# Performance work log

Hardware: AMD Instinct MI355X
Metric: run time of the kernel (lower is better)

## Reference

```python
import jax, jax.numpy as jnp
import numpy as np

THRESH = 1.0        # cif_weight_threshold
MAX_HIST = 10       # max_history
RELU_THRESH = 1.0   # relu_threshold (crelu clip)
NORM_SCALAR = 1.0   # normalize_scalar


def setup_inputs() -> dict:
    key = jax.random.key(0)
    k0, k1, k2 = jax.random.split(key, 3)
    B, T, H = 32, 2048, 256
    encoder_outputs = jax.random.normal(k0, (B, T, H), jnp.float32)
    mask = jnp.ones((B, 200, 1), jnp.float32)
    W1 = jax.random.normal(k1, (2 * H, 2 * H), jnp.float32) * 0.02
    b1 = jnp.zeros((2 * H,), jnp.float32)
    W2 = jax.random.normal(k2, (1, 2 * H), jnp.float32) * 0.02
    b2 = jnp.zeros((1,), jnp.float32)
    return {"encoder_outputs": encoder_outputs, "mask": mask,
            "W1": W1, "b1": b1, "W2": W2, "b2": b2, "is_training": 1}


def _cif_forward(x, mask, W1, b1, W2, b2, is_training):
    B, T, H = x.shape
    dt = x.dtype
    # number of non-zero (effective) frames per utterance
    first_pad = jnp.sum((jnp.sum(jnp.abs(x), -1) != 0.0).astype(jnp.int32), 1)  # [B]

    # ---- history chunk: mean over window [max(0, t-MAX_HIST), t); t==0 uses x[:,0] ----
    cs = jnp.concatenate([jnp.zeros((B, 1, H), dt), jnp.cumsum(x, axis=1)], axis=1)  # [B,T+1,H]
    t_idx = jnp.arange(T)
    start = jnp.maximum(0, t_idx - MAX_HIST)
    count = jnp.maximum(t_idx - start, 1).astype(dt)
    hist = (cs[:, t_idx, :] - cs[:, start, :]) / count[None, :, None]     # [B,T,H]
    hist = jnp.where((t_idx == 0)[None, :, None], x[:, 0:1, :], hist)

    # ---- weight prediction (two dense layers, crelu + clip) ----
    info = jnp.concatenate([x, x - hist], axis=-1)                        # [B,T,2H]
    h = jnp.einsum('btc,oc->bto', info, W1) + b1
    w = (jnp.einsum('btc,oc->bto', h, W2) + b2)[..., 0]                   # [B,T]
    w = jnp.clip(jax.nn.relu(w), None, RELU_THRESH)
    ori_weight = w
    sum_a = w.sum(1)

    if is_training:  # static python int; using_scaling=True, mask provided
        N = mask[:, :, 0].sum(-1) - 1.0
        scale = N / jnp.clip(sum_a, 1e-8)
        scale = jnp.where(sum_a == 0, jnp.zeros_like(sum_a), scale)
        w = scale[:, None] * w

    pad_mask = t_idx[None, :] > first_pad[:, None]                        # [B,T]
    w = jnp.where(pad_mask, 0.0, w)

    # ---- accumulate-and-fire scan ----
    def step(carry, inp):
        prev_w, prev_s = carry
        w_t, x_t = inp                                                    # [B], [B,H]
        fired = prev_w + w_t > THRESH
        remained = THRESH - prev_w
        new_w = jnp.where(fired, w_t - remained, w_t + prev_w)
        integ = prev_s + (1.0 - w_t)[:, None] * x_t
        new_s = jnp.where(fired[:, None], x_t, integ)
        fired_s = jnp.where(fired[:, None], integ, jnp.zeros_like(integ))
        return (new_w, new_s), (fired, fired_s)

    init = (jnp.zeros((B,), dt), x[:, 0, :])
    (fin_w, fin_s), (fired_flags, fired_states) = jax.lax.scan(
        step, init, (w.T, jnp.swapaxes(x, 0, 1)))

    fired_states = jnp.swapaxes(fired_states, 0, 1)                       # [B,T,H]
    fired_flag = fired_flags.T[:, :, None].astype(dt)                     # [B,T,1]
    fired_states = jnp.where(pad_mask[:, :, None], 0.0, fired_states)
    fired_states = jnp.concatenate([fired_states, fin_s[:, None, :]], 1)  # [B,T+1,H] (tail)

    # ---- compact fired states to the front (torch truncates to max fired len;
    #      here we keep fixed length T+1 and pad with zeros, which is a superset) ----
    L = T + 1
    fired_marks = (jnp.sum(jnp.abs(fired_states), -1) != 0.0).astype(jnp.int32)
    pos = jnp.cumsum(fired_marks, axis=1) - 1
    pos = jnp.where(fired_marks == 1, pos, L)  # out-of-bounds -> dropped
    cif = jnp.zeros((B, L, H), dt)
    cif = cif.at[jnp.arange(B)[:, None], pos].set(fired_states, mode='drop')

    not_padding_after_cif = (jnp.sum(jnp.abs(cif), -1) != 0.0).astype(jnp.int32)
    norm = jnp.linalg.norm(cif, axis=-1, keepdims=True)
    cif = NORM_SCALAR * cif / jnp.maximum(norm, 1e-12)  # F.normalize(p=2)
    return cif, ori_weight, fired_flag, not_padding_after_cif, sum_a


def reference(encoder_outputs, mask, W1, b1, W2, b2, is_training):
    return _cif_forward(encoder_outputs, mask, W1, b1, W2, b2, is_training)
```

## Files before the change

### kernel.cpp

```cpp
#include <hip/hip_runtime.h>

#define B_ 32
#define T_ 2048
#define H_ 256
#define L_ 2049

__device__ inline double waveReduceD(double v) {
#pragma unroll
  for (int off = 32; off > 0; off >>= 1) v += __shfl_xor(v, off, 64);
  return v;
}

typedef float vfloat4 __attribute__((ext_vector_type(4)));
__device__ inline void nt_store4(float4 v, float* p) {
  vfloat4 t;
  t.x = v.x; t.y = v.y; t.z = v.z; t.w = v.w;
  __builtin_nontemporal_store(t, (vfloat4*)p);
}

__global__ void __launch_bounds__(256) k0_fold(
    const float* __restrict__ W1, const float* __restrict__ b1,
    const float* __restrict__ W2, const float* __restrict__ b2,
    double* __restrict__ vd, double* __restrict__ c0) {
  __shared__ double s_p[8][32];
  int tid = threadIdx.x;
  int cl = tid & 31, sl = tid >> 5;
  int c = blockIdx.x * 32 + cl;
  double acc = 0.0;
#pragma unroll 8
  for (int o = sl * 64; o < sl * 64 + 64; ++o)
    acc += (double)W2[o] * (double)W1[o * 512 + c];
  s_p[sl][cl] = acc;
  __syncthreads();
  if (sl == 0) {
    double v = 0.0;
#pragma unroll
    for (int i = 0; i < 8; ++i) v += s_p[i][cl];
    vd[c] = v;
  }
  if (blockIdx.x == 0) {
    __shared__ double red[256];
    double p = (double)W2[tid] * (double)b1[tid] +
               (double)W2[tid + 256] * (double)b1[tid + 256];
    red[tid] = p;
    __syncthreads();
    for (int s = 128; s > 0; s >>= 1) {
      if (tid < s) red[tid] += red[tid + s];
      __syncthreads();
    }
    if (tid == 0) c0[0] = red[0] + (double)b2[0];
  }
}

__global__ void __launch_bounds__(256) k1_rowdots(
    const float* __restrict__ x, const double* __restrict__ vd,
    double* __restrict__ d1, double* __restrict__ d2, float* __restrict__ absS) {
  int wave = threadIdx.x >> 6, lane = threadIdx.x & 63;
  long row0 = ((long)blockIdx.x * 4 + wave) * 4;
  const float4* xr = (const float4*)(x + row0 * H_);
  float4 x0 = xr[lane];
  float4 x1 = xr[lane + 64];
  float4 x2 = xr[lane + 128];
  float4 x3 = xr[lane + 192];
  int base = lane * 4;
  double vb0 = vd[256 + base + 0], vb1 = vd[256 + base + 1],
         vb2 = vd[256 + base + 2], vb3 = vd[256 + base + 3];
  double va0 = vd[base + 0] + vb0, va1 = vd[base + 1] + vb1,
         va2 = vd[base + 2] + vb2, va3 = vd[base + 3] + vb3;
  double p10 = (double)x0.x * va0 + (double)x0.y * va1 + (double)x0.z * va2 + (double)x0.w * va3;
  double p20 = (double)x0.x * vb0 + (double)x0.y * vb1 + (double)x0.z * vb2 + (double)x0.w * vb3;
  double p11 = (double)x1.x * va0 + (double)x1.y * va1 + (double)x1.z * va2 + (double)x1.w * va3;
  double p21 = (double)x1.x * vb0 + (double)x1.y * vb1 + (double)x1.z * vb2 + (double)x1.w * vb3;
  double p12 = (double)x2.x * va0 + (double)x2.y * va1 + (double)x2.z * va2 + (double)x2.w * va3;
  double p22 = (double)x2.x * vb0 + (double)x2.y * vb1 + (double)x2.z * vb2 + (double)x2.w * vb3;
  double p13 = (double)x3.x * va0 + (double)x3.y * va1 + (double)x3.z * va2 + (double)x3.w * va3;
  double p23 = (double)x3.x * vb0 + (double)x3.y * vb1 + (double)x3.z * vb2 + (double)x3.w * vb3;
  bool n0 = (x0.x != 0.0f) || (x0.y != 0.0f) || (x0.z != 0.0f) || (x0.w != 0.0f);
  bool n1 = (x1.x != 0.0f) || (x1.y != 0.0f) || (x1.z != 0.0f) || (x1.w != 0.0f);
  bool n2 = (x2.x != 0.0f) || (x2.y != 0.0f) || (x2.z != 0.0f) || (x2.w != 0.0f);
  bool n3 = (x3.x != 0.0f) || (x3.y != 0.0f) || (x3.z != 0.0f) || (x3.w != 0.0f);
  unsigned long long b0 = __ballot(n0), b1_ = __ballot(n1),
                     b2_ = __ballot(n2), b3 = __ballot(n3);
#pragma unroll
  for (int off = 32; off > 0; off >>= 1) {
    p10 += __shfl_xor(p10, off, 64);
    p20 += __shfl_xor(p20, off, 64);
    p11 += __shfl_xor(p11, off, 64);
    p21 += __shfl_xor(p21, off, 64);
    p12 += __shfl_xor(p12, off, 64);
    p22 += __shfl_xor(p22, off, 64);
    p13 += __shfl_xor(p13, off, 64);
    p23 += __shfl_xor(p23, off, 64);
  }
  if (lane == 0)       { d1[row0 + 0] = p10; d2[row0 + 0] = p20; absS[row0 + 0] = b0  ? 1.0f : 0.0f; }
  else if (lane == 16) { d1[row0 + 1] = p11; d2[row0 + 1] = p21; absS[row0 + 1] = b1_ ? 1.0f : 0.0f; }
  else if (lane == 32) { d1[row0 + 2] = p12; d2[row0 + 2] = p22; absS[row0 + 2] = b2_ ? 1.0f : 0.0f; }
  else if (lane == 48) { d1[row0 + 3] = p13; d2[row0 + 3] = p23; absS[row0 + 3] = b3  ? 1.0f : 0.0f; }
}

__global__ void __launch_bounds__(256) k2_weights(
    const double* __restrict__ d1, const double* __restrict__ d2,
    const float* __restrict__ absS, const float* __restrict__ mask,
    const int* __restrict__ is_tr, const double* __restrict__ c0p,
    float* __restrict__ o_ori, float* __restrict__ o_sa, float* __restrict__ o_ff,
    float* __restrict__ wsc, int* __restrict__ fireT,
    int* __restrict__ nAllArr, int* __restrict__ nUnmArr) {
  __shared__ double s_P[T_];
  __shared__ double s_tot[4];
  __shared__ double s_red[4][3];
  __shared__ double s_tot2[4];
  __shared__ double s_mtot[4];
  __shared__ int s_int[2];
  int b = blockIdx.x, tid = threadIdx.x;
  int lane = tid & 63, wv = tid >> 6;
  int t0 = tid * 8;
  const double* d1b = d1 + (long)b * T_;
  const double* d2b = d2 + (long)b * T_;
  const float* asb = absS + (long)b * T_;
  double c0 = c0p[0];

  double r2[8];
  {
    double run2 = 0.0;
#pragma unroll
    for (int k = 0; k < 8; ++k) { run2 += d2b[t0 + k]; r2[k] = run2; }
    double sc2 = run2;
#pragma unroll
    for (int off = 1; off < 64; off <<= 1) {
      double n = __shfl_up(sc2, off, 64);
      if (lane >= off) sc2 += n;
    }
    if (lane == 63) s_tot[wv] = sc2;
    __syncthreads();
    double base2 = 0.0;
    for (int i = 0; i < wv; ++i) base2 += s_tot[i];
    double e2 = base2 + (sc2 - run2);
#pragma unroll
    for (int k = 0; k < 8; ++k) s_P[t0 + k] = e2 + r2[k];
  }
  __syncthreads();

  double wd[8];
  double sa = 0.0, fpc = 0.0;
#pragma unroll
  for (int k = 0; k < 8; ++k) {
    int t = t0 + k;
    double wvv;
    if (t == 0) {
      wvv = d1b[0] - s_P[0] + c0;
    } else {
      int start = t - 10; if (start < 0) start = 0;
      double ws_ = s_P[t - 1] - (start > 0 ? s_P[start - 1] : 0.0);
      wvv = d1b[t] - ws_ / (double)(t - start) + c0;
    }
    wvv = wvv < 0.0 ? 0.0 : (wvv > 1.0 ? 1.0 : wvv);
    wd[k] = wvv;
    sa += wvv;
    fpc += (asb[t] != 0.0f) ? 1.0 : 0.0;
  }
  {
    float4* ov = (float4*)(o_ori + (long)b * T_ + t0);
    ov[0] = make_float4((float)wd[0], (float)wd[1], (float)wd[2], (float)wd[3]);
    ov[1] = make_float4((float)wd[4], (float)wd[5], (float)wd[6], (float)wd[7]);
  }
  double ms = (tid < 200) ? (double)mask[(long)b * 200 + tid] : 0.0;
  double sar = waveReduceD(sa), fpr = waveReduceD(fpc), msr = waveReduceD(ms);
  if (lane == 0) { s_red[wv][0] = sar; s_red[wv][1] = fpr; s_red[wv][2] = msr; }
  __syncthreads();
  double sumA = s_red[0][0] + s_red[1][0] + s_red[2][0] + s_red[3][0];
  double fpD  = s_red[0][1] + s_red[1][1] + s_red[2][1] + s_red[3][1];
  double maskSum = s_red[0][2] + s_red[1][2] + s_red[2][2] + s_red[3][2];
  if (tid == 0) o_sa[b] = (float)sumA;
  int firstPad = (int)(fpD + 0.5);
  double scale;
  if (is_tr[0] != 0) {
    scale = (sumA == 0.0) ? 0.0 : (maskSum - 1.0) / (sumA > 1e-8 ? sumA : 1e-8);
  } else {
    scale = 1.0;
  }

  double a[8], r[8];
  double run = 0.0;
#pragma unroll
  for (int k = 0; k < 8; ++k) {
    int t = t0 + k;
    double av = wd[k] * scale;
    if (t > firstPad) av = 0.0;
    a[k] = av;
    run += av; r[k] = run;
  }
  {
    float4* wvv = (float4*)(wsc + (long)b * T_ + t0);
    wvv[0] = make_float4((float)a[0], (float)a[1], (float)a[2], (float)a[3]);
    wvv[1] = make_float4((float)a[4], (float)a[5], (float)a[6], (float)a[7]);
  }
  double sc = run;
#pragma unroll
  for (int off = 1; off < 64; off <<= 1) {
    double n = __shfl_up(sc, off, 64);
    if (lane >= off) sc += n;
  }
  if (lane == 63) s_tot2[wv] = sc;
  __syncthreads();
  double base = 0.0;
  for (int i = 0; i < wv; ++i) base += s_tot2[i];
  double e = base + (sc - run);

  double m[8];
  double mn = 1e300;
#pragma unroll
  for (int k = 0; k < 8; ++k) {
    double S = e + r[k];
    double kp = ceil(S - 1.0); if (kp < 0.0) kp = 0.0;
    double D = kp - (double)(t0 + k);
    mn = fmin(mn, D);
    m[k] = mn;
  }
  double scm = mn;
#pragma unroll
  for (int off = 1; off < 64; off <<= 1) {
    double n = __shfl_up(scm, off, 64);
    if (lane >= off) scm = fmin(scm, n);
  }
  double exw = __shfl_up(scm, 1, 64);
  if (lane == 0) exw = 1e300;
  if (lane == 63) s_mtot[wv] = scm;
  __syncthreads();
  double mbase = 1e300;
  for (int i = 0; i < wv; ++i) mbase = fmin(mbase, s_mtot[i]);
  double Mexcl = fmin(mbase, exw);

  float flags[8];
  int Cp = (t0 - 1) + (int)fmin(1.0, Mexcl);
#pragma unroll
  for (int k = 0; k < 8; ++k) {
    int t = t0 + k;
    double Mk = fmin(Mexcl, m[k]);
    int C = t + (int)fmin(1.0, Mk);
    bool fired = C > Cp;
    flags[k] = fired ? 1.0f : 0.0f;
    if (fired) fireT[(long)b * T_ + (C - 1)] = t;
    if (t == firstPad) s_int[0] = C;
    Cp = C;
  }
  {
    float4* fv = (float4*)(o_ff + (long)b * T_ + t0);
    fv[0] = make_float4(flags[0], flags[1], flags[2], flags[3]);
    fv[1] = make_float4(flags[4], flags[5], flags[6], flags[7]);
  }
  if (tid == 255) s_int[1] = Cp;
  __syncthreads();
  if (tid == 0) {
    int nA = s_int[1];
    nAllArr[b] = nA;
    nUnmArr[b] = (firstPad >= T_) ? nA : s_int[0];
  }
}

__global__ void __launch_bounds__(256) k4_rows(
    const float* __restrict__ x, const float* __restrict__ wsc,
    const int* __restrict__ fireT,
    const int* __restrict__ nAllArr, const int* __restrict__ nUnmArr,
    float* __restrict__ cif, float* __restrict__ notpad) {
  int wave = threadIdx.x >> 6, lane = threadIdx.x & 63;
  int pos = blockIdx.x * 4 + wave;
  int b = blockIdx.y;
  if (pos >= L_) return;
  int nA = nAllArr[b], nU = nUnmArr[b];
  float* crow = cif + ((long)b * L_ + pos) * H_ + lane * 4;
  if (pos > nU) {
    nt_store4(make_float4(0.0f, 0.0f, 0.0f, 0.0f), crow);
    if (lane == 0) notpad[(long)b * L_ + pos] = 0.0f;
    return;
  }
  const int* ftb = fireT + (long)b * T_;
  int hi, anchor, lo;
  if (pos < nU) {
    hi = ftb[pos];
    anchor = (pos == 0) ? 0 : ftb[pos - 1];
    lo = (pos == 0) ? 0 : anchor + 1;
  } else {
    hi = T_ - 1;
    anchor = (nA == 0) ? 0 : ftb[nA - 1];
    lo = (nA == 0) ? 0 : anchor + 1;
  }
  const float* xb = x + (long)b * T_ * H_;
  float4 acc = ((const float4*)(xb + (long)anchor * H_))[lane];
  float4 acc2 = make_float4(0.0f, 0.0f, 0.0f, 0.0f);
  const float* wb = wsc + (long)b * T_;
  int u = lo;
  for (; u + 1 <= hi; u += 2) {
    float f0 = 1.0f - wb[u];
    float f1 = 1.0f - wb[u + 1];
    float4 xv0 = ((const float4*)(xb + (long)u * H_))[lane];
    float4 xv1 = ((const float4*)(xb + (long)(u + 1) * H_))[lane];
    acc.x += f0 * xv0.x;  acc.y += f0 * xv0.y;
    acc.z += f0 * xv0.z;  acc.w += f0 * xv0.w;
    acc2.x += f1 * xv1.x; acc2.y += f1 * xv1.y;
    acc2.z += f1 * xv1.z; acc2.w += f1 * xv1.w;
  }
  if (u <= hi) {
    float f = 1.0f - wb[u];
    float4 xv = ((const float4*)(xb + (long)u * H_))[lane];
    acc.x += f * xv.x; acc.y += f * xv.y; acc.z += f * xv.z; acc.w += f * xv.w;
  }
  acc.x += acc2.x; acc.y += acc2.y; acc.z += acc2.z; acc.w += acc2.w;
  float ss = acc.x * acc.x + acc.y * acc.y + acc.z * acc.z + acc.w * acc.w;
#pragma unroll
  for (int off = 32; off > 0; off >>= 1) ss += __shfl_xor(ss, off, 64);
  float inv = 1.0f / fmaxf(sqrtf(ss), 1e-12f);
  nt_store4(make_float4(acc.x * inv, acc.y * inv, acc.z * inv, acc.w * inv), crow);
  if (lane == 0) notpad[(long)b * L_ + pos] = 1.0f;
}

extern "C" void kernel_launch(void* const* d_in, const int* in_sizes, int n_in,
                              void* d_out, int out_size, void* d_ws, size_t ws_size,
                              hipStream_t stream) {
  const float* x    = (const float*)d_in[0];
  const float* mask = (const float*)d_in[1];
  const float* W1   = (const float*)d_in[2];
  const float* b1   = (const float*)d_in[3];
  const float* W2   = (const float*)d_in[4];
  const float* b2   = (const float*)d_in[5];
  const int*   istr = (const int*)d_in[6];

  float* out = (float*)d_out;
  float* o_cif = out;
  float* o_ori = o_cif + (size_t)B_ * L_ * H_;
  float* o_ff  = o_ori + (size_t)B_ * T_;
  float* o_np  = o_ff  + (size_t)B_ * T_;
  float* o_sa  = o_np  + (size_t)B_ * L_;

  char* w = (char*)d_ws;
  double* vd   = (double*)w; w += 512 * 8;
  double* c0   = (double*)w; w += 8;
  double* d1   = (double*)w; w += (size_t)B_ * T_ * 8;
  double* d2   = (double*)w; w += (size_t)B_ * T_ * 8;
  float* absS  = (float*)w;  w += (size_t)B_ * T_ * 4;
  float* wsc   = (float*)w;  w += (size_t)B_ * T_ * 4;
  int* fireT   = (int*)w;    w += (size_t)B_ * T_ * 4;
  int* nAllA   = (int*)w;    w += B_ * 4;
  int* nUnmA   = (int*)w;    w += B_ * 4;

  k0_fold<<<16, 256, 0, stream>>>(W1, b1, W2, b2, vd, c0);
  k1_rowdots<<<(B_ * T_) / 16, 256, 0, stream>>>(x, vd, d1, d2, absS);
  k2_weights<<<B_, 256, 0, stream>>>(d1, d2, absS, mask, istr, c0,
                                     o_ori, o_sa, o_ff, wsc, fireT,
                                     nAllA, nUnmA);
  k4_rows<<<dim3((L_ + 3) / 4, B_), 256, 0, stream>>>(
      x, wsc, fireT, nAllA, nUnmA, o_cif, o_np);
}
```

Before: 152.0 us.

## Restructure row-dot kernel to 16-lane row groups with register-cached weights

The row-dot kernel now gives each row to a group of 16 threads, each handling 16 contiguous floats. Each thread caches its 32 folded-weight doubles in registers and reuses them across 4 rows, where before every wave reloaded weights for every set of 4 rows. The cross-lane reduction is cut from 6 to 4 shuffle levels, and the block count drops by 4x. The fold kernel also splits its accumulation into two chains to expose more ILP. The cost is higher register pressure from 32 double registers per thread, and the per-thread x loads are less coalesced (64-byte chunks per lane).

```diff
diff --git a/kernel.cpp b/kernel.cpp
--- a/kernel.cpp
+++ b/kernel.cpp
@@ -26,11 +26,13 @@
   int tid = threadIdx.x;
   int cl = tid & 31, sl = tid >> 5;
   int c = blockIdx.x * 32 + cl;
-  double acc = 0.0;
-#pragma unroll 8
-  for (int o = sl * 64; o < sl * 64 + 64; ++o)
-    acc += (double)W2[o] * (double)W1[o * 512 + c];
-  s_p[sl][cl] = acc;
+  double acc0 = 0.0, acc1 = 0.0;
+#pragma unroll 4
+  for (int o = sl * 64; o < sl * 64 + 64; o += 2) {
+    acc0 += (double)W2[o] * (double)W1[o * 512 + c];
+    acc1 += (double)W2[o + 1] * (double)W1[(o + 1) * 512 + c];
+  }
+  s_p[sl][cl] = acc0 + acc1;
   __syncthreads();
   if (sl == 0) {
     double v = 0.0;
@@ -55,47 +57,48 @@
 __global__ void __launch_bounds__(256) k1_rowdots(
     const float* __restrict__ x, const double* __restrict__ vd,
     double* __restrict__ d1, double* __restrict__ d2, float* __restrict__ absS) {
-  int wave = threadIdx.x >> 6, lane = threadIdx.x & 63;
-  long row0 = ((long)blockIdx.x * 4 + wave) * 4;
-  const float4* xr = (const float4*)(x + row0 * H_);
-  float4 x0 = xr[lane];
-  float4 x1 = xr[lane + 64];
-  float4 x2 = xr[lane + 128];
-  float4 x3 = xr[lane + 192];
-  int base = lane * 4;
-  double vb0 = vd[256 + base + 0], vb1 = vd[256 + base + 1],
-         vb2 = vd[256 + base + 2], vb3 = vd[256 + base + 3];
-  double va0 = vd[base + 0] + vb0, va1 = vd[base + 1] + vb1,
-         va2 = vd[base + 2] + vb2, va3 = vd[base + 3] + vb3;
-  double p10 = (double)x0.x * va0 + (double)x0.y * va1 + (double)x0.z * va2 + (double)x0.w * va3;
-  double p20 = (double)x0.x * vb0 + (double)x0.y * vb1 + (double)x0.z * vb2 + (double)x0.w * vb3;
-  double p11 = (double)x1.x * va0 + (double)x1.y * va1 + (double)x1.z * va2 + (double)x1.w * va3;
-  double p21 = (double)x1.x * vb0 + (double)x1.y * vb1 + (double)x1.z * vb2 + (double)x1.w * vb3;
-  double p12 = (double)x2.x * va0 + (double)x2.y * va1 + (double)x2.z * va2 + (double)x2.w * va3;
-  double p22 = (double)x2.x * vb0 + (double)x2.y * vb1 + (double)x2.z * vb2 + (double)x2.w * vb3;
-  double p13 = (double)x3.x * va0 + (double)x3.y * va1 + (double)x3.z * va2 + (double)x3.w * va3;
-  double p23 = (double)x3.x * vb0 + (double)x3.y * vb1 + (double)x3.z * vb2 + (double)x3.w * vb3;
-  bool n0 = (x0.x != 0.0f) || (x0.y != 0.0f) || (x0.z != 0.0f) || (x0.w != 0.0f);
-  bool n1 = (x1.x != 0.0f) || (x1.y != 0.0f) || (x1.z != 0.0f) || (x1.w != 0.0f);
-  bool n2 = (x2.x != 0.0f) || (x2.y != 0.0f) || (x2.z != 0.0f) || (x2.w != 0.0f);
-  bool n3 = (x3.x != 0.0f) || (x3.y != 0.0f) || (x3.z != 0.0f) || (x3.w != 0.0f);
-  unsigned long long b0 = __ballot(n0), b1_ = __ballot(n1),
-                     b2_ = __ballot(n2), b3 = __ballot(n3);
-#pragma unroll
-  for (int off = 32; off > 0; off >>= 1) {
-    p10 += __shfl_xor(p10, off, 64);
-    p20 += __shfl_xor(p20, off, 64);
-    p11 += __shfl_xor(p11, off, 64);
-    p21 += __shfl_xor(p21, off, 64);
-    p12 += __shfl_xor(p12, off, 64);
-    p22 += __shfl_xor(p22, off, 64);
-    p13 += __shfl_xor(p13, off, 64);
-    p23 += __shfl_xor(p23, off, 64);
-  }
-  if (lane == 0)       { d1[row0 + 0] = p10; d2[row0 + 0] = p20; absS[row0 + 0] = b0  ? 1.0f : 0.0f; }
-  else if (lane == 16) { d1[row0 + 1] = p11; d2[row0 + 1] = p21; absS[row0 + 1] = b1_ ? 1.0f : 0.0f; }
-  else if (lane == 32) { d1[row0 + 2] = p12; d2[row0 + 2] = p22; absS[row0 + 2] = b2_ ? 1.0f : 0.0f; }
-  else if (lane == 48) { d1[row0 + 3] = p13; d2[row0 + 3] = p23; absS[row0 + 3] = b3  ? 1.0f : 0.0f; }
+  int tid = threadIdx.x;
+  int s = tid & 15;
+  int slot = tid >> 4;
+  long rowBase = (long)blockIdx.x * 64;
+
+  double v12[16], v2v[16];
+#pragma unroll
+  for (int k = 0; k < 16; ++k) {
+    double bv = vd[256 + s * 16 + k];
+    v2v[k] = bv;
+    v12[k] = vd[s * 16 + k] + bv;
+  }
+
+#pragma unroll
+  for (int i = 0; i < 4; ++i) {
+    long row = rowBase + slot * 4 + i;
+    const float4* xr = (const float4*)(x + row * H_ + s * 16);
+    float4 a0 = xr[0], a1 = xr[1], a2 = xr[2], a3 = xr[3];
+    float e[16];
+    *(float4*)(e + 0) = a0; *(float4*)(e + 4) = a1;
+    *(float4*)(e + 8) = a2; *(float4*)(e + 12) = a3;
+    double p1 = 0.0, p2 = 0.0;
+    bool nz = false;
+#pragma unroll
+    for (int k = 0; k < 16; ++k) {
+      p1 += (double)e[k] * v12[k];
+      p2 += (double)e[k] * v2v[k];
+      nz |= (e[k] != 0.0f);
+    }
+    float nzf = nz ? 1.0f : 0.0f;
+#pragma unroll
+    for (int off = 1; off < 16; off <<= 1) {
+      p1 += __shfl_xor(p1, off, 64);
+      p2 += __shfl_xor(p2, off, 64);
+      nzf += __shfl_xor(nzf, off, 64);
+    }
+    if (s == 0) {
+      d1[row] = p1;
+      d2[row] = p2;
+      absS[row] = (nzf > 0.0f) ? 1.0f : 0.0f;
+    }
+  }
 }
 
 __global__ void __launch_bounds__(256) k2_weights(
@@ -343,7 +346,7 @@
   int* nUnmA   = (int*)w;    w += B_ * 4;
 
   k0_fold<<<16, 256, 0, stream>>>(W1, b1, W2, b2, vd, c0);
-  k1_rowdots<<<(B_ * T_) / 16, 256, 0, stream>>>(x, vd, d1, d2, absS);
+  k1_rowdots<<<(B_ * T_) / 64, 256, 0, stream>>>(x, vd, d1, d2, absS);
   k2_weights<<<B_, 256, 0, stream>>>(d1, d2, absS, mask, istr, c0,
                                      o_ori, o_sa, o_ff, wsc, fireT,
                                      nAllA, nUnmA);
```

After: 153.1 us. About the same (+0.7%).
